# Optimization experiments

Measured on AMD Instinct MI355X. Metric: run time of the kernel, lower is better.

Reference implementation:

```python
import jax, jax.numpy as jnp
import numpy as np

N_NODES = 100000
N_EDGES = 3200000
D = 128
K = 10
NITER = 10


def kmeans(x, K=K, Niter=NITER):
    # c init = first K points, Lloyd iterations (matches the LazyTensor KMeans math)
    N, Dm = x.shape
    c = x[:K, :]
    cl = jnp.zeros((N,), dtype=jnp.int32)
    for _ in range(Niter):
        # argmin_j ||x_i - c_j||^2 == argmin_j (-2 x_i.c_j + ||c_j||^2)
        d = -2.0 * (x @ c.T) + jnp.sum(c * c, axis=-1)  # [N, K]
        cl = jnp.argmin(d, axis=1)
        counts = jax.ops.segment_sum(jnp.ones((N,), x.dtype), cl, num_segments=K)
        sums = jax.ops.segment_sum(x, cl, num_segments=K)
        c = sums / jnp.maximum(counts, 1.0)[:, None]  # guard empty clusters
    return cl, c


def scatter_softmax(scores, seg_ids, num_segments):
    # numerically-stable softmax over edges grouped by seg_ids (torch_geometric.utils.softmax)
    seg_max = jax.ops.segment_max(scores, seg_ids, num_segments=num_segments)
    shifted = jnp.exp(scores - seg_max[seg_ids])
    seg_sum = jax.ops.segment_sum(shifted, seg_ids, num_segments=num_segments)
    return shifted / (seg_sum[seg_ids] + 1e-16)


def setup_inputs() -> dict:
    key = jax.random.key(0)
    k1, k2, k3, k4, k5 = jax.random.split(key, 5)
    x = jax.random.normal(k1, (N_NODES, D), dtype=jnp.float32)
    edge = jax.random.randint(k2, (2, N_EDGES), 0, N_NODES, dtype=jnp.int64)
    # xavier_normal gain 1.414 on [D, D]: std = gain * sqrt(2 / (fan_in + fan_out))
    std = 1.414 * np.sqrt(2.0 / (D + D))
    WQ = jax.random.normal(k3, (D, D), dtype=jnp.float32) * std
    WV = jax.random.normal(k4, (D, D), dtype=jnp.float32) * std
    WK = jax.random.normal(k5, (D, D), dtype=jnp.float32) * std
    return {"x": x, "edge": edge, "WQ": WQ, "WV": WV, "WK": WK}


def reference(x, edge, WQ, WV, WK):
    attention_norm_idx = 0
    alloc, centroids = kmeans(x)                      # [N], [K, D]
    q = centroids @ WQ                                 # [K, D]
    v = centroids @ WV                                 # [K, D]
    prods = (q @ v.T) / jnp.sqrt(jnp.asarray(WK.shape[1], x.dtype))  # [K, K]
    centroid_attention = jax.nn.softmax(prods, axis=1)
    src_c = alloc[edge[0, :]]                          # [E]
    dst_c = alloc[edge[1, :]]                          # [E]
    edge_attention = centroid_attention[src_c, dst_c]  # [E] gather
    attention = scatter_softmax(edge_attention, edge[attention_norm_idx], N_NODES)
    return attention
```

## Files before the change

kernel.cpp:

```cpp
#include <hip/hip_runtime.h>

#define NN 100000
#define NE 3200000
#define DD 128
#define KC 10
#define NITER 10
#define NBK 1024
#define NPAIR (NN / 2)
#define NB4 (NPAIR / 4)
#define NE4 (NE / 4)

template <int CTRL, int RM>
__device__ __forceinline__ float dppadd(float v) {
  int t = __builtin_amdgcn_update_dpp(0, __builtin_bit_cast(int, v), CTRL, RM,
                                      0xF, true);
  return v + __builtin_bit_cast(float, t);
}

__device__ __forceinline__ float halfsum_tail(float v) {
  v = dppadd<0x111, 0xF>(v);
  v = dppadd<0x112, 0xF>(v);
  v = dppadd<0x114, 0xF>(v);
  v = dppadd<0x118, 0xF>(v);
  v = dppadd<0x142, 0xA>(v);
  return v;
}
__device__ __forceinline__ int bcast31i(int v) {
  return __builtin_amdgcn_ds_swizzle(v, 0x3E0);
}

__global__ __launch_bounds__(256, 2) void k_iter6(
    const float* __restrict__ x, const float* __restrict__ csrc,
    float* __restrict__ partial, float* __restrict__ cntpart,
    unsigned char* __restrict__ cl8, int last) {
  __shared__ float cs[KC][DD];
  __shared__ float wsum[4][KC][DD];
  __shared__ float wcnt[4][KC];
  const int tid = threadIdx.x;
  float* wsf = (float*)wsum;
  for (int i = tid; i < KC * DD; i += 256) ((float*)cs)[i] = csrc[i];
  for (int i = tid; i < 4 * KC * DD; i += 256) wsf[i] = 0.f;
  __syncthreads();
  const int w = tid >> 6, lane = tid & 63, half = lane >> 5, hl = lane & 31;

  float4 cfrag[KC];
  float bias[KC];
#pragma unroll
  for (int j = 0; j < KC; ++j) {
    const float4 c4 = *(const float4*)&cs[j][hl * 4];
    cfrag[j] = c4;
    bias[j] = -0.5f * (c4.x * c4.x + c4.y * c4.y + c4.z * c4.z + c4.w * c4.w);
  }
  unsigned int cntlo = 0, cnthi = 0;

  float* const wrow = &wsum[w][0][hl * 4];
  const float4* __restrict__ x4 = (const float4*)x;
  const int g = blockIdx.x * 4 + w;
  const int stride = NBK * 4;

  float4 vA[4], vB[4];

  auto compute = [&](const float4* v, int B) {
#pragma unroll
    for (int u = 0; u < 4; ++u) {
      const int row = 8 * B + 2 * u + half;
      float d[KC];
#pragma unroll
      for (int j = 0; j < KC; ++j)
        d[j] = bias[j] + v[u].x * cfrag[j].x + v[u].y * cfrag[j].y +
               v[u].z * cfrag[j].z + v[u].w * cfrag[j].w;
#pragma unroll
      for (int j = 0; j < KC; ++j) d[j] = halfsum_tail(d[j]);
      int best = 0;
      float bd = d[0];
#pragma unroll
      for (int j = 1; j < KC; ++j) {
        if (d[j] > bd) { bd = d[j]; best = j; }
      }
      const int bown = bcast31i(best);
      const int bother = __shfl_xor(bown, 32);
      const unsigned sh = 6u * (unsigned)bown;
      cntlo += (bown < 5) ? (1u << sh) : 0u;
      cnthi += (bown >= 5) ? (1u << (sh - 30u)) : 0u;
      if (last && hl == 0) cl8[row] = (unsigned char)bown;

      if (bown == bother) {
        float4 vs;
        vs.x = v[u].x + __shfl_xor(v[u].x, 32);
        vs.y = v[u].y + __shfl_xor(v[u].y, 32);
        vs.z = v[u].z + __shfl_xor(v[u].z, 32);
        vs.w = v[u].w + __shfl_xor(v[u].w, 32);
        if (half == 0) {
          float4 t = *(float4*)&wrow[bown * DD];
          t.x += vs.x; t.y += vs.y; t.z += vs.z; t.w += vs.w;
          *(float4*)&wrow[bown * DD] = t;
        }
      } else {
        float4 t = *(float4*)&wrow[bown * DD];
        t.x += v[u].x; t.y += v[u].y; t.z += v[u].z; t.w += v[u].w;
        *(float4*)&wrow[bown * DD] = t;
      }
    }
  };
  auto loadb = [&](float4* v, int B) {
    const size_t rb = (size_t)(8 * B) * 32;
#pragma unroll
    for (int u = 0; u < 4; ++u) v[u] = x4[rb + (size_t)(2 * u + half) * 32 + hl];
  };

  int B = g;
  if (B < NB4) {
    loadb(vA, B);
    for (;;) {
      if (B + stride < NB4) loadb(vB, B + stride);
      compute(vA, B);
      B += stride;
      if (B >= NB4) break;
      if (B + stride < NB4) loadb(vA, B + stride);
      compute(vB, B);
      B += stride;
      if (B >= NB4) break;
    }
  }
  __syncthreads();
  for (int i = tid; i < KC * DD; i += 256)
    partial[(size_t)blockIdx.x * (KC * DD) + i] =
        wsf[i] + wsf[KC * DD + i] + wsf[2 * KC * DD + i] + wsf[3 * KC * DD + i];
  cntlo += __shfl_xor(cntlo, 32);
  cnthi += __shfl_xor(cnthi, 32);
  if (lane == 0) {
#pragma unroll
    for (int j = 0; j < 5; ++j) {
      wcnt[w][j] = (float)((cntlo >> (6 * j)) & 63u);
      wcnt[w][j + 5] = (float)((cnthi >> (6 * j)) & 63u);
    }
  }
  __syncthreads();
  if (tid < KC)
    cntpart[blockIdx.x * KC + tid] =
        wcnt[0][tid] + wcnt[1][tid] + wcnt[2][tid] + wcnt[3][tid];
}

__global__ __launch_bounds__(256) void k_update2(
    const float* __restrict__ partial, const float* __restrict__ cntpart,
    float* __restrict__ c) {
  const int j = blockIdx.x >> 4, q = blockIdx.x & 15;
  const int tid = threadIdx.x;
  __shared__ float creds[256];
  __shared__ float red2[32][8];
  float cf = 0.f;
#pragma unroll
  for (int m = 0; m < NBK / 256; ++m) cf += cntpart[(tid + 256 * m) * KC + j];
  creds[tid] = cf;
  __syncthreads();
  for (int s = 128; s > 0; s >>= 1) {
    if (tid < s) creds[tid] += creds[tid + s];
    __syncthreads();
  }
  const float denom = fmaxf(creds[0], 1.f);
  const int cc = tid & 7, r = tid >> 3;
  const int col = j * DD + q * 8 + cc;
  float s0 = 0.f;
#pragma unroll 8
  for (int m = 0; m < NBK / 32; ++m)
    s0 += partial[(size_t)(r + 32 * m) * (KC * DD) + col];
  red2[r][cc] = s0;
  __syncthreads();
  if (tid < 8) {
    float t = 0.f;
#pragma unroll
    for (int rr = 0; rr < 32; ++rr) t += red2[rr][tid];
    c[j * DD + q * 8 + tid] = t / denom;
  }
}

__global__ __launch_bounds__(DD) void k_qv(const float* __restrict__ c,
                                           const float* __restrict__ WQ,
                                           const float* __restrict__ WV,
                                           float* __restrict__ qv) {
  const int b = blockIdx.x;
  const int mat = b / KC, i = b % KC;
  const float* __restrict__ W = mat ? WV : WQ;
  __shared__ float cr[DD];
  const int k = threadIdx.x;
  cr[k] = c[i * DD + k];
  __syncthreads();
  float a = 0.f;
#pragma unroll 8
  for (int m = 0; m < DD; ++m) a += cr[m] * W[m * DD + k];
  qv[(size_t)mat * KC * DD + i * DD + k] = a;
}

__global__ __launch_bounds__(DD) void k_att(const float* __restrict__ qv,
                                            float* __restrict__ CA) {
  __shared__ float q[KC][DD + 2], v[KC][DD + 2], pr[KC][KC];
  const int tid = threadIdx.x;
  for (int i = 0; i < KC; ++i) {
    q[i][tid] = qv[i * DD + tid];
    v[i][tid] = qv[KC * DD + i * DD + tid];
  }
  __syncthreads();
  if (tid < KC * KC) {
    const int i = tid / KC, l = tid % KC;
    float acc = 0.f;
#pragma unroll 8
    for (int m = 0; m < DD; ++m) acc += q[i][m] * v[l][m];
    pr[i][l] = acc / sqrtf((float)DD);
  }
  __syncthreads();
  if (tid < KC) {
    float mx = pr[tid][0];
    for (int l = 1; l < KC; ++l) mx = fmaxf(mx, pr[tid][l]);
    float e[KC];
    float s = 0.f;
    for (int l = 0; l < KC; ++l) {
      e[l] = expf(pr[tid][l] - mx);
      s += e[l];
    }
    for (int l = 0; l < KC; ++l) CA[tid * KC + l] = e[l] / s;
  }
}

__global__ __launch_bounds__(256) void k_cnt(const int* __restrict__ e0,
                                             const int* __restrict__ e1,
                                             const unsigned char* __restrict__ cl8,
                                             int* __restrict__ cnt, int base) {
  const int i = base + blockIdx.x * 256 + threadIdx.x;
  if (i >= NE4) return;
  const int4 a = ((const int4*)e0)[i];
  const int4 b = ((const int4*)e1)[i];
  atomicAdd(&cnt[(size_t)a.x * KC + cl8[b.x]], 1);
  atomicAdd(&cnt[(size_t)a.y * KC + cl8[b.y]], 1);
  atomicAdd(&cnt[(size_t)a.z * KC + cl8[b.z]], 1);
  atomicAdd(&cnt[(size_t)a.w * KC + cl8[b.w]], 1);
}

__global__ __launch_bounds__(256) void k_tab2(
    const unsigned char* __restrict__ cl8, const int* __restrict__ cnt,
    const float* __restrict__ CA, float* __restrict__ den) {
  __shared__ float cas[KC * KC];
  __shared__ float rm[KC];
  if (threadIdx.x < KC * KC) cas[threadIdx.x] = CA[threadIdx.x];
  __syncthreads();
  if (threadIdx.x < KC) {
    float m = cas[threadIdx.x * KC];
    for (int l = 1; l < KC; ++l) m = fmaxf(m, cas[threadIdx.x * KC + l]);
    rm[threadIdx.x] = m;
  }
  __syncthreads();
  const int n = blockIdx.x * 256 + threadIdx.x;
  if (n >= NN) return;
  const int s = cl8[n];
  const float m = rm[s];
  float dsum = 0.f;
#pragma unroll
  for (int j = 0; j < KC; ++j) {
    const int cj = cnt[(size_t)n * KC + j];
    dsum += (float)cj * expf(cas[s * KC + j] - m);
  }
  den[n] = dsum;
}

__global__ __launch_bounds__(256) void k_gather2(
    const int* __restrict__ e0, const int* __restrict__ e1,
    const unsigned char* __restrict__ cl8, const float* __restrict__ CA,
    const float* __restrict__ den, float* __restrict__ out) {
  __shared__ float cas[KC * KC];
  __shared__ float rm[KC];
  if (threadIdx.x < KC * KC) cas[threadIdx.x] = CA[threadIdx.x];
  __syncthreads();
  if (threadIdx.x < KC) {
    float m = cas[threadIdx.x * KC];
    for (int l = 1; l < KC; ++l) m = fmaxf(m, cas[threadIdx.x * KC + l]);
    rm[threadIdx.x] = m;
  }
  __syncthreads();
  const int i = blockIdx.x * 256 + threadIdx.x;
  const int4 a = ((const int4*)e0)[i];
  const int4 b = ((const int4*)e1)[i];
  float4 r;
  {
    const int s = cl8[a.x];
    r.x = expf(cas[s * KC + cl8[b.x]] - rm[s]) / (den[a.x] + 1e-16f);
  }
  {
    const int s = cl8[a.y];
    r.y = expf(cas[s * KC + cl8[b.y]] - rm[s]) / (den[a.y] + 1e-16f);
  }
  {
    const int s = cl8[a.z];
    r.z = expf(cas[s * KC + cl8[b.z]] - rm[s]) / (den[a.z] + 1e-16f);
  }
  {
    const int s = cl8[a.w];
    r.w = expf(cas[s * KC + cl8[b.w]] - rm[s]) / (den[a.w] + 1e-16f);
  }
  ((float4*)out)[i] = r;
}

extern "C" void kernel_launch(void* const* d_in, const int* in_sizes, int n_in,
                              void* d_out, int out_size, void* d_ws,
                              size_t ws_size, hipStream_t stream) {
  const float* x = (const float*)d_in[0];
  const int* edge = (const int*)d_in[1];
  const float* WQ = (const float*)d_in[2];
  const float* WV = (const float*)d_in[3];
  float* out = (float*)d_out;
  const int* e0 = edge;
  const int* e1 = edge + NE;

  float* ws = (float*)d_ws;
  float* c = ws;
  float* CA = ws + 1280;
  float* qv = ws + 1392;
  float* den = qv + 2 * KC * DD;
  float* partial = den + NN;
  float* cntpart = partial + (size_t)NBK * KC * DD;
  int* cnt = (int*)(cntpart + NBK * KC);
  unsigned char* cl8 = (unsigned char*)(cnt + (size_t)NN * KC);

  hipMemsetAsync(cnt, 0, (size_t)NN * KC * sizeof(int), stream);

  for (int it = 0; it < NITER; ++it) {
    const float* csrc = (it == 0) ? x : c;
    k_iter6<<<NBK, 256, 0, stream>>>(x, csrc, partial, cntpart, cl8,
                                     it == NITER - 1);
    k_update2<<<KC * 16, 256, 0, stream>>>(partial, cntpart, c);
  }
  k_qv<<<2 * KC, DD, 0, stream>>>(c, WQ, WV, qv);
  k_att<<<1, DD, 0, stream>>>(qv, CA);
  const int TOT_BLKS = (NE4 + 255) / 256;
  const int QB8 = (TOT_BLKS + 7) / 8;
  for (int q = 0; q < 8; ++q) {
    const int nb = (q < 7) ? QB8 : (TOT_BLKS - 7 * QB8);
    k_cnt<<<nb, 256, 0, stream>>>(e0, e1, cl8, cnt, q * QB8 * 256);
  }
  k_tab2<<<(NN + 255) / 256, 256, 0, stream>>>(cl8, cnt, CA, den);
  k_gather2<<<NE4 / 256, 256, 0, stream>>>(e0, e1, cl8, CA, den, out);
}
```

Before: 502.1 us.

## Partition k-means rows per XCD and pack denominator with cluster id

The k-means iteration kernel now assigns each of the 8 XCDs (chosen by blockIdx & 7) a contiguous slice of the row-pair blocks, so each XCD's L2 keeps re-reading its own part of x across iterations instead of an interleaved mix. Separately, the per-node denominator is stored as a float2 together with the source node's cluster id, so the edge gather kernel fetches both with one random access instead of two separate gathers (cl8 and den). The cost is a wider den buffer and a float-to-int conversion of the cluster id, and the XCD mapping assumes round-robin block dispatch.

```diff
diff --git a/kernel.cpp b/kernel.cpp
--- a/kernel.cpp
+++ b/kernel.cpp
@@ -9,6 +9,7 @@
 #define NPAIR (NN / 2)
 #define NB4 (NPAIR / 4)
 #define NE4 (NE / 4)
+#define NWX 512
 
 template <int CTRL, int RM>
 __device__ __forceinline__ float dppadd(float v) {
@@ -55,8 +56,11 @@
 
   float* const wrow = &wsum[w][0][hl * 4];
   const float4* __restrict__ x4 = (const float4*)x;
-  const int g = blockIdx.x * 4 + w;
-  const int stride = NBK * 4;
+
+  const int xcd = blockIdx.x & 7;
+  const int wk = (blockIdx.x >> 3) * 4 + w;
+  const int bs = (xcd * NB4) / 8;
+  const int be = ((xcd + 1) * NB4) / 8;
 
   float4 vA[4], vB[4];
 
@@ -108,18 +112,18 @@
     for (int u = 0; u < 4; ++u) v[u] = x4[rb + (size_t)(2 * u + half) * 32 + hl];
   };
 
-  int B = g;
-  if (B < NB4) {
+  int B = bs + wk;
+  if (B < be) {
     loadb(vA, B);
     for (;;) {
-      if (B + stride < NB4) loadb(vB, B + stride);
+      if (B + NWX < be) loadb(vB, B + NWX);
       compute(vA, B);
-      B += stride;
-      if (B >= NB4) break;
-      if (B + stride < NB4) loadb(vA, B + stride);
+      B += NWX;
+      if (B >= be) break;
+      if (B + NWX < be) loadb(vA, B + NWX);
       compute(vB, B);
-      B += stride;
-      if (B >= NB4) break;
+      B += NWX;
+      if (B >= be) break;
     }
   }
   __syncthreads();
@@ -237,7 +241,7 @@
 
 __global__ __launch_bounds__(256) void k_tab2(
     const unsigned char* __restrict__ cl8, const int* __restrict__ cnt,
-    const float* __restrict__ CA, float* __restrict__ den) {
+    const float* __restrict__ CA, float2* __restrict__ den2) {
   __shared__ float cas[KC * KC];
   __shared__ float rm[KC];
   if (threadIdx.x < KC * KC) cas[threadIdx.x] = CA[threadIdx.x];
@@ -258,13 +262,13 @@
     const int cj = cnt[(size_t)n * KC + j];
     dsum += (float)cj * expf(cas[s * KC + j] - m);
   }
-  den[n] = dsum;
+  den2[n] = float2{dsum, (float)s};
 }
 
 __global__ __launch_bounds__(256) void k_gather2(
     const int* __restrict__ e0, const int* __restrict__ e1,
     const unsigned char* __restrict__ cl8, const float* __restrict__ CA,
-    const float* __restrict__ den, float* __restrict__ out) {
+    const float2* __restrict__ den2, float* __restrict__ out) {
   __shared__ float cas[KC * KC];
   __shared__ float rm[KC];
   if (threadIdx.x < KC * KC) cas[threadIdx.x] = CA[threadIdx.x];
@@ -280,20 +284,24 @@
   const int4 b = ((const int4*)e1)[i];
   float4 r;
   {
-    const int s = cl8[a.x];
-    r.x = expf(cas[s * KC + cl8[b.x]] - rm[s]) / (den[a.x] + 1e-16f);
+    const float2 dc = den2[a.x];
+    const int s = (int)dc.y;
+    r.x = expf(cas[s * KC + cl8[b.x]] - rm[s]) / (dc.x + 1e-16f);
   }
   {
-    const int s = cl8[a.y];
-    r.y = expf(cas[s * KC + cl8[b.y]] - rm[s]) / (den[a.y] + 1e-16f);
+    const float2 dc = den2[a.y];
+    const int s = (int)dc.y;
+    r.y = expf(cas[s * KC + cl8[b.y]] - rm[s]) / (dc.x + 1e-16f);
   }
   {
-    const int s = cl8[a.z];
-    r.z = expf(cas[s * KC + cl8[b.z]] - rm[s]) / (den[a.z] + 1e-16f);
+    const float2 dc = den2[a.z];
+    const int s = (int)dc.y;
+    r.z = expf(cas[s * KC + cl8[b.z]] - rm[s]) / (dc.x + 1e-16f);
   }
   {
-    const int s = cl8[a.w];
-    r.w = expf(cas[s * KC + cl8[b.w]] - rm[s]) / (den[a.w] + 1e-16f);
+    const float2 dc = den2[a.w];
+    const int s = (int)dc.y;
+    r.w = expf(cas[s * KC + cl8[b.w]] - rm[s]) / (dc.x + 1e-16f);
   }
   ((float4*)out)[i] = r;
 }
@@ -313,8 +321,8 @@
   float* c = ws;
   float* CA = ws + 1280;
   float* qv = ws + 1392;
-  float* den = qv + 2 * KC * DD;
-  float* partial = den + NN;
+  float2* den2 = (float2*)(qv + 2 * KC * DD);
+  float* partial = (float*)(den2 + NN);
   float* cntpart = partial + (size_t)NBK * KC * DD;
   int* cnt = (int*)(cntpart + NBK * KC);
   unsigned char* cl8 = (unsigned char*)(cnt + (size_t)NN * KC);
@@ -335,6 +343,6 @@
     const int nb = (q < 7) ? QB8 : (TOT_BLKS - 7 * QB8);
     k_cnt<<<nb, 256, 0, stream>>>(e0, e1, cl8, cnt, q * QB8 * 256);
   }
-  k_tab2<<<(NN + 255) / 256, 256, 0, stream>>>(cl8, cnt, CA, den);
-  k_gather2<<<NE4 / 256, 256, 0, stream>>>(e0, e1, cl8, CA, den, out);
-}
+  k_tab2<<<(NN + 255) / 256, 256, 0, stream>>>(cl8, cnt, CA, den2);
+  k_gather2<<<NE4 / 256, 256, 0, stream>>>(e0, e1, cl8, CA, den2, out);
+}
```

After: 496.0 us. No clear change (-1.2%).
